# Optimization experiments

Measured on AMD Instinct MI355X. Metric: run time of the kernel, lower is better.

## Reference

```python
import jax, jax.numpy as jnp
import numpy as np
from jax import lax

B, H_IMG, W_IMG = 512, 812, 40
HID = 128
NUM_CLASSES = 12
LSTM_IN = 32 * ((W_IMG - 5) // 2 + 1)  # 32 channels * 18 = 576


def setup_inputs() -> dict:
    key = jax.random.key(0)
    ks = jax.random.split(key, 20)
    s = 0.05
    inp = {
        "x": jax.random.normal(ks[0], (B, 1, H_IMG, W_IMG), jnp.float32),
        "conv_w": jax.random.normal(ks[1], (32, 1, 20, 5), jnp.float32) * s,
        "conv_b": jax.random.normal(ks[2], (32,), jnp.float32) * s,
        "Wih0": jax.random.normal(ks[3], (4 * HID, LSTM_IN), jnp.float32) * s,
        "Whh0": jax.random.normal(ks[4], (4 * HID, HID), jnp.float32) * s,
        "bih0": jax.random.normal(ks[5], (4 * HID,), jnp.float32) * s,
        "bhh0": jax.random.normal(ks[6], (4 * HID,), jnp.float32) * s,
        "Wih1": jax.random.normal(ks[7], (4 * HID, HID), jnp.float32) * s,
        "Whh1": jax.random.normal(ks[8], (4 * HID, HID), jnp.float32) * s,
        "bih1": jax.random.normal(ks[9], (4 * HID,), jnp.float32) * s,
        "bhh1": jax.random.normal(ks[10], (4 * HID,), jnp.float32) * s,
        "W_att": jax.random.normal(ks[11], (HID, HID), jnp.float32) * s,
        "b_att": jax.random.normal(ks[12], (HID,), jnp.float32) * s,
        "v_att": jax.random.normal(ks[13], (HID,), jnp.float32) * s,
        "W1": jax.random.normal(ks[14], (64, HID), jnp.float32) * s,
        "b1": jax.random.normal(ks[15], (64,), jnp.float32) * s,
        "W2": jax.random.normal(ks[16], (NUM_CLASSES, 64), jnp.float32) * s,
        "b2": jax.random.normal(ks[17], (NUM_CLASSES,), jnp.float32) * s,
    }
    return inp


def _lstm_layer(seq, Wih, Whh, bih, bhh):
    # seq: (T, B, I); PyTorch gate order i, f, g, o
    T, Bn, _ = seq.shape
    Hd = Whh.shape[1]
    x_proj = jnp.einsum('tbi,gi->tbg', seq, Wih) + bih + bhh  # (T,B,4H)

    def step(carry, xg):
        h, c = carry
        g = xg + h @ Whh.T
        i, f, gg, o = jnp.split(g, 4, axis=-1)
        c = jax.nn.sigmoid(f) * c + jax.nn.sigmoid(i) * jnp.tanh(gg)
        h = jax.nn.sigmoid(o) * jnp.tanh(c)
        return (h, c), h

    init = (jnp.zeros((Bn, Hd), seq.dtype), jnp.zeros((Bn, Hd), seq.dtype))
    _, hs = lax.scan(step, init, x_proj)
    return hs  # (T,B,H)


def _forward(x, conv_w, conv_b, Wih0, Whh0, bih0, bhh0, Wih1, Whh1, bih1, bhh1,
             W_att, b_att, v_att, W1, b1, W2, b2):
    # Conv2d(1->32, k=(20,5), s=(8,2)) + ReLU
    y = lax.conv_general_dilated(x, conv_w, (8, 2), 'VALID',
                                 dimension_numbers=('NCHW', 'OIHW', 'NCHW'))
    y = jax.nn.relu(y + conv_b[None, :, None, None])  # (B,32,T,W')
    b, c, t, w = y.shape
    # permute(0,2,3,1).view(b,t,-1).permute(1,0,2) -> (T,B,W'*32)
    seq = jnp.transpose(y, (2, 0, 3, 1)).reshape(t, b, w * c)
    # 2-layer LSTM (inter-layer dropout=0.2 inactive at eval)
    h1 = _lstm_layer(seq, Wih0, Whh0, bih0, bhh0)
    h2 = _lstm_layer(h1, Wih1, Whh1, bih1, bhh1)
    # additive attention pooling over time
    squish = jnp.tanh(jnp.einsum('tbh,hk->tbk', h2, W_att) + b_att)  # (T,B,H)
    attn = jnp.einsum('tbh,h->tb', squish, v_att)                     # (T,B)
    w_att_n = jax.nn.softmax(attn, axis=0)                            # softmax over T
    pooled = jnp.einsum('tb,tbh->bh', w_att_n, h2)                    # (B,H)
    # dnn1 -> (dropout inactive at eval) -> output
    hdn = pooled @ W1.T + b1
    return hdn @ W2.T + b2  # (B,num_classes)


def reference(x, conv_w, conv_b, Wih0, Whh0, bih0, bhh0, Wih1, Whh1, bih1, bhh1,
              W_att, b_att, v_att, W1, b1, W2, b2):
    return _forward(x, conv_w, conv_b, Wih0, Whh0, bih0, bhh0, Wih1, Whh1,
                    bih1, bhh1, W_att, b_att, v_att, W1, b1, W2, b2)
```

## Files before the change

kernel.cpp:

```cpp
#include <hip/hip_runtime.h>
#include <stdint.h>


#define T_STEPS 100
#define BATCH   512
#define HIDD    128
#define GATES   512
#define LSTMIN  576
#define HIMG    812
#define WIMG    40

typedef __attribute__((ext_vector_type(8))) short bf16x8;
typedef __attribute__((ext_vector_type(4))) float f32x4;
typedef __attribute__((ext_vector_type(2))) __fp16 f16x2;

__device__ inline unsigned short f2bf(float f) {
  unsigned u = __float_as_uint(f);
  unsigned r = (u + 0x7fffu + ((u >> 16) & 1u)) >> 16;
  return (unsigned short)r;
}
__device__ inline float bf2f(unsigned short b) {
  return __uint_as_float(((unsigned)b) << 16);
}
__device__ inline float fsigm(float x) {
  float e = __expf(-x);
  return __builtin_amdgcn_rcpf(1.f + e);
}
__device__ inline float ftanh(float x) {
  float e = __expf(2.f * x);
  return (e - 1.f) * __builtin_amdgcn_rcpf(e + 1.f);
}
__device__ inline void lds_barrier() {
  asm volatile("s_waitcnt lgkmcnt(0)" ::: "memory");
  __builtin_amdgcn_s_barrier();
}
__device__ inline void full_barrier() {
  asm volatile("s_waitcnt vmcnt(0) lgkmcnt(0)" ::: "memory");
  __builtin_amdgcn_s_barrier();
}
__device__ inline void wait_flag(const int* fp, int need) {
  if ((threadIdx.x & 63) == 0) {
    int v = __hip_atomic_load(fp, __ATOMIC_ACQUIRE, __HIP_MEMORY_SCOPE_AGENT);
    while (v < need) {
      __builtin_amdgcn_s_sleep(2);
      v = __hip_atomic_load(fp, __ATOMIC_ACQUIRE, __HIP_MEMORY_SCOPE_AGENT);
    }
  }
}

__global__ void prep_kernel(const float* __restrict__ Wih0, const float* __restrict__ Whh0,
                            const float* __restrict__ Wih1, const float* __restrict__ Whh1,
                            const float* __restrict__ Watt, const float* __restrict__ convw,
                            const float* __restrict__ bih0, const float* __restrict__ bhh0,
                            const float* __restrict__ bih1, const float* __restrict__ bhh1,
                            unsigned short* __restrict__ wih0b, unsigned short* __restrict__ whh0b,
                            unsigned short* __restrict__ wih1b, unsigned short* __restrict__ whh1b,
                            unsigned short* __restrict__ wattb, f16x2* __restrict__ wpair,
                            float* __restrict__ bias0, float* __restrict__ bias1,
                            int* __restrict__ flags) {
  int tid = blockIdx.x * blockDim.x + threadIdx.x;
  int stride = gridDim.x * blockDim.x;
  for (int i = tid; i < GATES * LSTMIN; i += stride) wih0b[i] = f2bf(Wih0[i]);
  for (int i = tid; i < GATES * HIDD; i += stride) whh0b[i] = f2bf(Whh0[i]);
  for (int i = tid; i < GATES * HIDD; i += stride) wih1b[i] = f2bf(Wih1[i]);
  for (int i = tid; i < GATES * HIDD; i += stride) whh1b[i] = f2bf(Whh1[i]);
  for (int i = tid; i < HIDD * HIDD; i += stride) {
    int j = i >> 7, k = i & 127;
    wattb[i] = f2bf(Watt[k * HIDD + j]);
  }
  for (int i = tid; i < 50 * 32; i += stride) {
    int k2 = i >> 5, c = i & 31;
    int kh2 = k2 / 5, kw = k2 % 5;
    float lo = convw[c * 100 + (2 * kh2) * 5 + kw];
    float hi = convw[c * 100 + (2 * kh2 + 1) * 5 + kw];
    wpair[i] = __builtin_amdgcn_cvt_pkrtz(lo, hi);
  }
  for (int i = tid; i < GATES; i += stride) bias0[i] = bih0[i] + bhh0[i];
  for (int i = tid; i < GATES; i += stride) bias1[i] = bih1[i] + bhh1[i];
  for (int i = tid; i < 32; i += stride) flags[i] = 0;
}

__global__ __launch_bounds__(256) void conv_kernel(const float* __restrict__ x,
                                                   const f16x2* __restrict__ wpair,
                                                   const float* __restrict__ convb,
                                                   unsigned short* __restrict__ seq) {
  __shared__ f16x2 imgp[106 * WIMG];
  const int b = blockIdx.x;
  const int chunk = blockIdx.y;
  const int t0 = chunk * 25;
  const float* src = x + (size_t)b * (HIMG * WIMG) + (size_t)(8 * t0) * WIMG;
  for (int i = threadIdx.x; i < 106 * WIMG; i += 256) {
    int r2 = i / WIMG, c = i % WIMG;
    float lo = src[(2 * r2) * WIMG + c];
    float hi = src[(2 * r2 + 1) * WIMG + c];
    imgp[i] = __builtin_amdgcn_cvt_pkrtz(lo, hi);
  }
  __syncthreads();
  for (int p = threadIdx.x; p < 450; p += 256) {
    int tl = p / 18, wp = p % 18;
    int t = t0 + tl;
    float acc[32];
#pragma unroll
    for (int c = 0; c < 32; ++c) acc[c] = 0.f;
    const f16x2* ibase = imgp + (4 * tl) * WIMG + 2 * wp;
#pragma unroll 2
    for (int kh2 = 0; kh2 < 10; ++kh2) {
#pragma unroll
      for (int kw = 0; kw < 5; ++kw) {
        f16x2 iv = ibase[kh2 * WIMG + kw];
        const f16x2* wk = wpair + (kh2 * 5 + kw) * 32;
#pragma unroll
        for (int c = 0; c < 32; ++c)
          acc[c] = __builtin_amdgcn_fdot2(iv, wk[c], acc[c], false);
      }
    }
    unsigned short* o = seq + ((size_t)(t * BATCH + b)) * LSTMIN + wp * 32;
#pragma unroll
    for (int c = 0; c < 32; ++c) {
      float v = acc[c] + convb[c];
      o[c] = f2bf(v > 0.f ? v : 0.f);
    }
  }
}

template <int KDIM>
__global__ __launch_bounds__(256) void gemm_xp_kernel(const unsigned short* __restrict__ A,
                                                      const unsigned short* __restrict__ Bw,
                                                      const float* __restrict__ bias,
                                                      unsigned short* __restrict__ Xp) {
  __shared__ __align__(16) unsigned short As[128 * 32];
  __shared__ __align__(16) unsigned short Bs[128 * 32];
  const int tid = threadIdx.x;
  const int lane = tid & 63;
  const int w = tid >> 6;
  const int col16 = lane & 15;
  const int q = lane >> 4;
  const int n0 = blockIdx.x * 128;
  const int m0 = blockIdx.y * 128;
  const int wm = (w & 1) * 64;
  const int wn = (w >> 1) * 64;
  f32x4 acc[4][4] = {};
  const int r = tid >> 2;
  const int sw = ((tid & 3) ^ (r & 3)) * 8;
  const unsigned wslot = (unsigned)w * 512;
  const unsigned short* ga = A + (size_t)(m0 + r) * KDIM + sw;
  const unsigned short* gb = Bw + (size_t)(n0 + r) * KDIM + sw;
  for (int k0 = 0; k0 < KDIM; k0 += 32) {
    __syncthreads();
    __builtin_amdgcn_global_load_lds((const __attribute__((address_space(1))) void*)(ga + k0),
                                     (__attribute__((address_space(3))) void*)(As + wslot), 16, 0, 0);
    __builtin_amdgcn_global_load_lds((const __attribute__((address_space(1))) void*)(ga + k0 + (size_t)64 * KDIM),
                                     (__attribute__((address_space(3))) void*)(As + wslot + 2048), 16, 0, 0);
    __builtin_amdgcn_global_load_lds((const __attribute__((address_space(1))) void*)(gb + k0),
                                     (__attribute__((address_space(3))) void*)(Bs + wslot), 16, 0, 0);
    __builtin_amdgcn_global_load_lds((const __attribute__((address_space(1))) void*)(gb + k0 + (size_t)64 * KDIM),
                                     (__attribute__((address_space(3))) void*)(Bs + wslot + 2048), 16, 0, 0);
    __syncthreads();
    bf16x8 af[4], bv[4];
#pragma unroll
    for (int i = 0; i < 4; ++i) {
      int ra = wm + i * 16 + col16;
      af[i] = *(const bf16x8*)(As + ra * 32 + ((q ^ (ra & 3)) * 8));
      int rb2 = wn + i * 16 + col16;
      bv[i] = *(const bf16x8*)(Bs + rb2 * 32 + ((q ^ (rb2 & 3)) * 8));
    }
#pragma unroll
    for (int i = 0; i < 4; ++i)
#pragma unroll
      for (int j = 0; j < 4; ++j)
        acc[i][j] = __builtin_amdgcn_mfma_f32_16x16x32_bf16(af[i], bv[j], acc[i][j], 0, 0, 0);
  }
#pragma unroll
  for (int ct = 0; ct < 4; ++ct) {
    int n = n0 + wn + ct * 16 + col16;
    float bvv = bias[n];
    int wS = (n >> 4) & 7;
    int ntS = n >> 7;
    int c16S = n & 15;
#pragma unroll
    for (int rt = 0; rt < 4; ++rt) {
      int m = m0 + wm + rt * 16 + q * 4;
      int t = m >> 9;
      int bb = m & 511;
      int blk = bb >> 4;
      int r16 = bb & 15;
      ushort4 u;
      u.x = f2bf(acc[rt][ct][0] + bvv);
      u.y = f2bf(acc[rt][ct][1] + bvv);
      u.z = f2bf(acc[rt][ct][2] + bvv);
      u.w = f2bf(acc[rt][ct][3] + bvv);
      size_t tile = (((size_t)t * 32 + blk) * 8 + wS) * 4 + ntS;
      *(ushort4*)(Xp + tile * 256 + c16S * 16 + r16) = u;
    }
  }
}

__global__ __launch_bounds__(512, 2) void scan_pipe_kernel(
    const unsigned short* __restrict__ Xp0, const unsigned short* __restrict__ Whh0,
    const unsigned short* __restrict__ Wih1, const float* __restrict__ bias1,
    unsigned short* __restrict__ Xp1, const unsigned short* __restrict__ Whh1,
    unsigned short* __restrict__ hout, int* __restrict__ flags) {
  __shared__ __align__(16) unsigned short hb[2][16 * 136];
  const int tid = threadIdx.x;
  const int lane = tid & 63;
  const int w = tid >> 6;
  const int col16 = lane & 15;
  const int q = lane >> 4;
  const bool producer = blockIdx.x < 32;
  const int blk = producer ? (int)blockIdx.x : (int)blockIdx.x - 32;
  const int rb = blk * 16;
  const int hc = w * 16 + col16;
  const int srow = tid >> 5;
  const int scol = (tid & 31) * 4;
  int* flagp = flags + blk;

  if (producer) {
    bf16x8 bfrag[4][4], bfrag2[4][4];
    const unsigned short* xpb[4];
    unsigned short* xob[4];
    float biasn[4];
#pragma unroll
    for (int nt = 0; nt < 4; ++nt) {
      int cn = nt * HIDD + hc;
#pragma unroll
      for (int ks = 0; ks < 4; ++ks) {
        bfrag[nt][ks] = *(const bf16x8*)(Whh0 + (size_t)cn * HIDD + ks * 32 + q * 8);
        bfrag2[nt][ks] = *(const bf16x8*)(Wih1 + (size_t)cn * HIDD + ks * 32 + q * 8);
      }
      biasn[nt] = bias1[cn];
      size_t tile = (((size_t)blk) * 8 + w) * 4 + nt;
      xpb[nt] = Xp0 + tile * 256 + col16 * 16 + q * 4;
      xob[nt] = Xp1 + tile * 256 + col16 * 16 + q * 4;
    }
    uint2 xb[2][4];
#pragma unroll
    for (int nt = 0; nt < 4; ++nt) xb[0][nt] = *(const uint2*)(xpb[nt]);
#pragma unroll
    for (int nt = 0; nt < 4; ++nt) xb[1][nt] = *(const uint2*)(xpb[nt] + GATES * BATCH);
    for (int i = tid; i < 2 * 16 * 136; i += 512) hb[0][i] = 0;
    float cst[4] = {0.f, 0.f, 0.f, 0.f};
    lds_barrier();

#pragma unroll 4
    for (int t = 0; t < T_STEPS; ++t) {
      const int pb = (t & 1) ^ 1;
      bf16x8 af[4];
#pragma unroll
      for (int ks = 0; ks < 4; ++ks)
        af[ks] = *(const bf16x8*)(hb[pb] + col16 * 136 + ks * 32 + q * 8);
      const int s = t & 1;
      uint2 xv[4];
#pragma unroll
      for (int nt = 0; nt < 4; ++nt) xv[nt] = xb[s][nt];
      if (t + 2 < T_STEPS) {
#pragma unroll
        for (int nt = 0; nt < 4; ++nt)
          xb[s][nt] = *(const uint2*)(xpb[nt] + (size_t)(t + 2) * (GATES * BATCH));
      }
      f32x4 acc[4];
#pragma unroll
      for (int nt = 0; nt < 4; ++nt) {
        acc[nt][0] = __uint_as_float(xv[nt].x << 16);
        acc[nt][1] = __uint_as_float(xv[nt].x & 0xffff0000u);
        acc[nt][2] = __uint_as_float(xv[nt].y << 16);
        acc[nt][3] = __uint_as_float(xv[nt].y & 0xffff0000u);
      }
#pragma unroll
      for (int ks = 0; ks < 4; ++ks)
#pragma unroll
        for (int nt = 0; nt < 4; ++nt)
          acc[nt] = __builtin_amdgcn_mfma_f32_16x16x32_bf16(af[ks], bfrag[nt][ks], acc[nt], 0, 0, 0);
      f32x4 acc2[4];
#pragma unroll
      for (int nt = 0; nt < 4; ++nt) acc2[nt] = f32x4{0.f, 0.f, 0.f, 0.f};
#pragma unroll
      for (int ks = 0; ks < 4; ++ks)
#pragma unroll
        for (int nt = 0; nt < 4; ++nt)
          acc2[nt] = __builtin_amdgcn_mfma_f32_16x16x32_bf16(af[ks], bfrag2[nt][ks], acc2[nt], 0, 0, 0);
      unsigned short hv[4];
#pragma unroll
      for (int rr = 0; rr < 4; ++rr) {
        float pi = acc[0][rr], pf = acc[1][rr];
        float pg = acc[2][rr], po = acc[3][rr];
        float cc = fsigm(pf) * cst[rr] + fsigm(pi) * ftanh(pg);
        cst[rr] = cc;
        hv[rr] = f2bf(fsigm(po) * ftanh(cc));
      }
      if (t > 0) {
#pragma unroll
        for (int nt = 0; nt < 4; ++nt) {
          ushort4 u;
          u.x = f2bf(acc2[nt][0] + biasn[nt]);
          u.y = f2bf(acc2[nt][1] + biasn[nt]);
          u.z = f2bf(acc2[nt][2] + biasn[nt]);
          u.w = f2bf(acc2[nt][3] + biasn[nt]);
          *(ushort4*)(xob[nt] + (size_t)(t - 1) * (GATES * BATCH)) = u;
        }
      }
#pragma unroll
      for (int rr = 0; rr < 4; ++rr)
        hb[t & 1][(q * 4 + rr) * 136 + hc] = hv[rr];
      if ((t & 3) == 3) {
        full_barrier();
        if (tid == 0)
          __hip_atomic_store(flagp, t, __ATOMIC_RELEASE, __HIP_MEMORY_SCOPE_AGENT);
      } else {
        lds_barrier();
      }
    }
    bf16x8 af[4];
#pragma unroll
    for (int ks = 0; ks < 4; ++ks)
      af[ks] = *(const bf16x8*)(hb[(T_STEPS - 1) & 1] + col16 * 136 + ks * 32 + q * 8);
    f32x4 acc2[4];
#pragma unroll
    for (int nt = 0; nt < 4; ++nt) acc2[nt] = f32x4{0.f, 0.f, 0.f, 0.f};
#pragma unroll
    for (int ks = 0; ks < 4; ++ks)
#pragma unroll
      for (int nt = 0; nt < 4; ++nt)
        acc2[nt] = __builtin_amdgcn_mfma_f32_16x16x32_bf16(af[ks], bfrag2[nt][ks], acc2[nt], 0, 0, 0);
#pragma unroll
    for (int nt = 0; nt < 4; ++nt) {
      ushort4 u;
      u.x = f2bf(acc2[nt][0] + biasn[nt]);
      u.y = f2bf(acc2[nt][1] + biasn[nt]);
      u.z = f2bf(acc2[nt][2] + biasn[nt]);
      u.w = f2bf(acc2[nt][3] + biasn[nt]);
      *(ushort4*)(xob[nt] + (size_t)(T_STEPS - 1) * (GATES * BATCH)) = u;
    }
    full_barrier();
    if (tid == 0)
      __hip_atomic_store(flagp, 100, __ATOMIC_RELEASE, __HIP_MEMORY_SCOPE_AGENT);
  } else {
    bf16x8 bfrag[4][4];
    const unsigned short* xpb[4];
#pragma unroll
    for (int nt = 0; nt < 4; ++nt) {
      int cn = nt * HIDD + hc;
#pragma unroll
      for (int ks = 0; ks < 4; ++ks)
        bfrag[nt][ks] = *(const bf16x8*)(Whh1 + (size_t)cn * HIDD + ks * 32 + q * 8);
      size_t tile = (((size_t)blk) * 8 + w) * 4 + nt;
      xpb[nt] = Xp1 + tile * 256 + col16 * 16 + q * 4;
    }
    for (int i = tid; i < 2 * 16 * 136; i += 512) hb[0][i] = 0;
    wait_flag(flagp, 6);
    uint2 xb[2][4];
#pragma unroll
    for (int nt = 0; nt < 4; ++nt) xb[0][nt] = *(const uint2*)(xpb[nt]);
#pragma unroll
    for (int nt = 0; nt < 4; ++nt) xb[1][nt] = *(const uint2*)(xpb[nt] + GATES * BATCH);
    float cst[4] = {0.f, 0.f, 0.f, 0.f};
    lds_barrier();

#pragma unroll 4
    for (int t = 0; t < T_STEPS; ++t) {
      if (t > 0 && (t & 3) == 0) {
        int need = t + 6;
        if (need > 100) need = 100;
        wait_flag(flagp, need);
      }
      const int pb = (t & 1) ^ 1;
      bf16x8 af[4];
#pragma unroll
      for (int ks = 0; ks < 4; ++ks)
        af[ks] = *(const bf16x8*)(hb[pb] + col16 * 136 + ks * 32 + q * 8);
      if (t > 0) {
        ushort4 hx = *(const ushort4*)(hb[pb] + srow * 136 + scol);
        *(ushort4*)(hout + ((size_t)((t - 1) * BATCH) + rb + srow) * HIDD + scol) = hx;
      }
      const int s = t & 1;
      uint2 xv[4];
#pragma unroll
      for (int nt = 0; nt < 4; ++nt) xv[nt] = xb[s][nt];
      if (t + 2 < T_STEPS) {
#pragma unroll
        for (int nt = 0; nt < 4; ++nt)
          xb[s][nt] = *(const uint2*)(xpb[nt] + (size_t)(t + 2) * (GATES * BATCH));
      }
      f32x4 acc[4];
#pragma unroll
      for (int nt = 0; nt < 4; ++nt) {
        acc[nt][0] = __uint_as_float(xv[nt].x << 16);
        acc[nt][1] = __uint_as_float(xv[nt].x & 0xffff0000u);
        acc[nt][2] = __uint_as_float(xv[nt].y << 16);
        acc[nt][3] = __uint_as_float(xv[nt].y & 0xffff0000u);
      }
#pragma unroll
      for (int ks = 0; ks < 4; ++ks)
#pragma unroll
        for (int nt = 0; nt < 4; ++nt)
          acc[nt] = __builtin_amdgcn_mfma_f32_16x16x32_bf16(af[ks], bfrag[nt][ks], acc[nt], 0, 0, 0);
      unsigned short hv[4];
#pragma unroll
      for (int rr = 0; rr < 4; ++rr) {
        float pi = acc[0][rr], pf = acc[1][rr];
        float pg = acc[2][rr], po = acc[3][rr];
        float cc = fsigm(pf) * cst[rr] + fsigm(pi) * ftanh(pg);
        cst[rr] = cc;
        hv[rr] = f2bf(fsigm(po) * ftanh(cc));
      }
#pragma unroll
      for (int rr = 0; rr < 4; ++rr)
        hb[t & 1][(q * 4 + rr) * 136 + hc] = hv[rr];
      lds_barrier();
    }
    ushort4 hx = *(const ushort4*)(hb[(T_STEPS - 1) & 1] + srow * 136 + scol);
    *(ushort4*)(hout + ((size_t)((T_STEPS - 1) * BATCH) + rb + srow) * HIDD + scol) = hx;
  }
}

__global__ __launch_bounds__(256) void gemm_att_kernel(const unsigned short* __restrict__ A,
                                                       const unsigned short* __restrict__ Bw,
                                                       const float* __restrict__ b_att,
                                                       const float* __restrict__ v_att,
                                                       float* __restrict__ scores) {
  __shared__ __align__(16) unsigned short As[128 * 32];
  __shared__ __align__(16) unsigned short Bs[128 * 32];
  __shared__ float s_red[128];
  const int tid = threadIdx.x;
  const int lane = tid & 63;
  const int w = tid >> 6;
  const int col16 = lane & 15;
  const int q = lane >> 4;
  const int m0 = blockIdx.y * 128;
  const int wm = (w & 1) * 64;
  const int wn = (w >> 1) * 64;
  f32x4 acc[4][4] = {};
  const int r = tid >> 2;
  const int sw = ((tid & 3) ^ (r & 3)) * 8;
  const unsigned wslot = (unsigned)w * 512;
  const unsigned short* ga = A + (size_t)(m0 + r) * HIDD + sw;
  const unsigned short* gb = Bw + (size_t)r * HIDD + sw;
  for (int k0 = 0; k0 < HIDD; k0 += 32) {
    __syncthreads();
    __builtin_amdgcn_global_load_lds((const __attribute__((address_space(1))) void*)(ga + k0),
                                     (__attribute__((address_space(3))) void*)(As + wslot), 16, 0, 0);
    __builtin_amdgcn_global_load_lds((const __attribute__((address_space(1))) void*)(ga + k0 + (size_t)64 * HIDD),
                                     (__attribute__((address_space(3))) void*)(As + wslot + 2048), 16, 0, 0);
    __builtin_amdgcn_global_load_lds((const __attribute__((address_space(1))) void*)(gb + k0),
                                     (__attribute__((address_space(3))) void*)(Bs + wslot), 16, 0, 0);
    __builtin_amdgcn_global_load_lds((const __attribute__((address_space(1))) void*)(gb + k0 + (size_t)64 * HIDD),
                                     (__attribute__((address_space(3))) void*)(Bs + wslot + 2048), 16, 0, 0);
    __syncthreads();
    bf16x8 af[4], bv[4];
#pragma unroll
    for (int i = 0; i < 4; ++i) {
      int ra = wm + i * 16 + col16;
      af[i] = *(const bf16x8*)(As + ra * 32 + ((q ^ (ra & 3)) * 8));
      int rb2 = wn + i * 16 + col16;
      bv[i] = *(const bf16x8*)(Bs + rb2 * 32 + ((q ^ (rb2 & 3)) * 8));
    }
#pragma unroll
    for (int i = 0; i < 4; ++i)
#pragma unroll
      for (int j = 0; j < 4; ++j)
        acc[i][j] = __builtin_amdgcn_mfma_f32_16x16x32_bf16(af[i], bv[j], acc[i][j], 0, 0, 0);
  }
  if (tid < 128) s_red[tid] = 0.f;
  float rs[4][4];
#pragma unroll
  for (int rt = 0; rt < 4; ++rt)
#pragma unroll
    for (int rr = 0; rr < 4; ++rr) rs[rt][rr] = 0.f;
#pragma unroll
  for (int ct = 0; ct < 4; ++ct) {
    int n = wn + ct * 16 + col16;
    float bvv = b_att[n], vv = v_att[n];
#pragma unroll
    for (int rt = 0; rt < 4; ++rt)
#pragma unroll
      for (int rr = 0; rr < 4; ++rr) {
        float xv2 = acc[rt][ct][rr] + bvv;
        float e = __expf(2.f * xv2);
        rs[rt][rr] += vv * (e - 1.f) * __builtin_amdgcn_rcpf(e + 1.f);
      }
  }
#pragma unroll
  for (int off = 1; off < 16; off <<= 1)
#pragma unroll
    for (int rt = 0; rt < 4; ++rt)
#pragma unroll
      for (int rr = 0; rr < 4; ++rr) rs[rt][rr] += __shfl_xor(rs[rt][rr], off, 64);
  __syncthreads();
  if (col16 == 0) {
#pragma unroll
    for (int rt = 0; rt < 4; ++rt)
#pragma unroll
      for (int rr = 0; rr < 4; ++rr)
        atomicAdd(&s_red[wm + rt * 16 + q * 4 + rr], rs[rt][rr]);
  }
  __syncthreads();
  if (tid < 128) scores[m0 + tid] = s_red[tid];
}

__global__ __launch_bounds__(128) void final_kernel(const float* __restrict__ scores,
                                                    const unsigned short* __restrict__ h2,
                                                    const float* __restrict__ W1, const float* __restrict__ b1,
                                                    const float* __restrict__ W2, const float* __restrict__ b2,
                                                    float* __restrict__ out) {
  const int b = blockIdx.x;
  const int tid = threadIdx.x;
  __shared__ float wj[T_STEPS];
  __shared__ float red[128];
  __shared__ float pooled[128];
  __shared__ float hdn[64];
  float sv = (tid < T_STEPS) ? scores[tid * BATCH + b] : -1e30f;
  red[tid] = sv;
  __syncthreads();
#pragma unroll
  for (int off = 64; off > 0; off >>= 1) {
    if (tid < off) red[tid] = fmaxf(red[tid], red[tid + off]);
    __syncthreads();
  }
  float mx = red[0];
  __syncthreads();
  float ev = (tid < T_STEPS) ? __expf(sv - mx) : 0.f;
  red[tid] = ev;
  __syncthreads();
#pragma unroll
  for (int off = 64; off > 0; off >>= 1) {
    if (tid < off) red[tid] += red[tid + off];
    __syncthreads();
  }
  float inv = 1.0f / red[0];
  if (tid < T_STEPS) wj[tid] = ev * inv;
  __syncthreads();
  float p = 0.f;
  for (int t = 0; t < T_STEPS; ++t)
    p += wj[t] * bf2f(h2[((size_t)(t * BATCH + b)) * HIDD + tid]);
  pooled[tid] = p;
  __syncthreads();
  if (tid < 64) {
    float a = b1[tid];
    for (int h = 0; h < 128; ++h) a = fmaf(W1[tid * 128 + h], pooled[h], a);
    hdn[tid] = a;
  }
  __syncthreads();
  if (tid < 12) {
    float a = b2[tid];
    for (int j = 0; j < 64; ++j) a = fmaf(W2[tid * 64 + j], hdn[j], a);
    out[b * 12 + tid] = a;
  }
}

extern "C" void kernel_launch(void* const* d_in, const int* in_sizes, int n_in,
                              void* d_out, int out_size, void* d_ws, size_t ws_size,
                              hipStream_t stream) {
  (void)in_sizes; (void)n_in; (void)out_size; (void)ws_size;
  const float* x      = (const float*)d_in[0];
  const float* conv_w = (const float*)d_in[1];
  const float* conv_b = (const float*)d_in[2];
  const float* Wih0   = (const float*)d_in[3];
  const float* Whh0   = (const float*)d_in[4];
  const float* bih0   = (const float*)d_in[5];
  const float* bhh0   = (const float*)d_in[6];
  const float* Wih1   = (const float*)d_in[7];
  const float* Whh1   = (const float*)d_in[8];
  const float* bih1   = (const float*)d_in[9];
  const float* bhh1   = (const float*)d_in[10];
  const float* W_att  = (const float*)d_in[11];
  const float* b_att  = (const float*)d_in[12];
  const float* v_att  = (const float*)d_in[13];
  const float* W1     = (const float*)d_in[14];
  const float* b1     = (const float*)d_in[15];
  const float* W2     = (const float*)d_in[16];
  const float* b2     = (const float*)d_in[17];

  char* ws = (char*)d_ws;
  size_t off = 0;
  auto carve = [&](size_t bytes) { char* p = ws + off; off += (bytes + 255) & ~(size_t)255; return p; };
  unsigned short* seq    = (unsigned short*)carve((size_t)T_STEPS * BATCH * LSTMIN * 2);
  unsigned short* xp0    = (unsigned short*)carve((size_t)T_STEPS * GATES * BATCH * 2);
  unsigned short* h2     = (unsigned short*)carve((size_t)T_STEPS * BATCH * HIDD * 2);
  float*          scores = (float*)carve((size_t)T_STEPS * BATCH * 4);
  unsigned short* wih0b  = (unsigned short*)carve((size_t)GATES * LSTMIN * 2);
  unsigned short* whh0b  = (unsigned short*)carve((size_t)GATES * HIDD * 2);
  unsigned short* wih1b  = (unsigned short*)carve((size_t)GATES * HIDD * 2);
  unsigned short* whh1b  = (unsigned short*)carve((size_t)GATES * HIDD * 2);
  unsigned short* wattb  = (unsigned short*)carve((size_t)HIDD * HIDD * 2);
  f16x2*          wpair  = (f16x2*)carve(50 * 32 * 4);
  float*          bias0  = (float*)carve(GATES * 4);
  float*          bias1  = (float*)carve(GATES * 4);
  int*            flags  = (int*)carve(32 * 4);
  unsigned short* xp1 = seq;

  prep_kernel<<<256, 256, 0, stream>>>(Wih0, Whh0, Wih1, Whh1, W_att, conv_w,
                                       bih0, bhh0, bih1, bhh1,
                                       wih0b, whh0b, wih1b, whh1b, wattb, wpair,
                                       bias0, bias1, flags);
  conv_kernel<<<dim3(512, 4), 256, 0, stream>>>(x, wpair, conv_b, seq);
  gemm_xp_kernel<LSTMIN><<<dim3(4, 400), 256, 0, stream>>>(seq, wih0b, bias0, xp0);
  scan_pipe_kernel<<<64, 512, 0, stream>>>(xp0, whh0b, wih1b, bias1, xp1, whh1b, h2, flags);
  gemm_att_kernel<<<dim3(1, 400), 256, 0, stream>>>(h2, wattb, b_att, v_att, scores);
  final_kernel<<<512, 128, 0, stream>>>(scores, h2, W1, b1, W2, b2, (float*)d_out);
}
```

Measured before the change: 412.5 us.

## Defer layer-1 projection stores and relax producer-consumer flag synchronization

The producer now holds each step's layer-1 input projection in registers and stores it one step later as relaxed atomics. Its periodic barrier waits with vmcnt(4) instead of draining every outstanding global op, so the flag publish no longer stalls on the newest stores. Flag acquire and release become relaxed with compiler fences, the consumer lag grows by one step, packed bf16 conversion is used, and launch bounds drop to one block per SM. The relaxed ordering depends on the vmcnt counting being right and risks subtle memory-visibility races.

```diff
diff --git a/kernel.cpp b/kernel.cpp
--- a/kernel.cpp
+++ b/kernel.cpp
@@ -13,12 +13,21 @@
 typedef __attribute__((ext_vector_type(8))) short bf16x8;
 typedef __attribute__((ext_vector_type(4))) float f32x4;
 typedef __attribute__((ext_vector_type(2))) __fp16 f16x2;
+typedef unsigned long long ull;
 
 __device__ inline unsigned short f2bf(float f) {
   unsigned u = __float_as_uint(f);
   unsigned r = (u + 0x7fffu + ((u >> 16) & 1u)) >> 16;
   return (unsigned short)r;
 }
+__device__ inline unsigned pk_bf16(float a, float b) {
+#if __has_builtin(__builtin_amdgcn_cvt_pk_bf16_f32)
+  auto r = __builtin_amdgcn_cvt_pk_bf16_f32(a, b);
+  return __builtin_bit_cast(unsigned, r);
+#else
+  return (unsigned)f2bf(a) | ((unsigned)f2bf(b) << 16);
+#endif
+}
 __device__ inline float bf2f(unsigned short b) {
   return __uint_as_float(((unsigned)b) << 16);
 }
@@ -34,18 +43,12 @@
   asm volatile("s_waitcnt lgkmcnt(0)" ::: "memory");
   __builtin_amdgcn_s_barrier();
 }
-__device__ inline void full_barrier() {
-  asm volatile("s_waitcnt vmcnt(0) lgkmcnt(0)" ::: "memory");
-  __builtin_amdgcn_s_barrier();
-}
-__device__ inline void wait_flag(const int* fp, int need) {
+__device__ inline void wait_flag(int* fp, int need) {
   if ((threadIdx.x & 63) == 0) {
-    int v = __hip_atomic_load(fp, __ATOMIC_ACQUIRE, __HIP_MEMORY_SCOPE_AGENT);
-    while (v < need) {
+    while (__hip_atomic_load(fp, __ATOMIC_RELAXED, __HIP_MEMORY_SCOPE_AGENT) < need)
       __builtin_amdgcn_s_sleep(2);
-      v = __hip_atomic_load(fp, __ATOMIC_ACQUIRE, __HIP_MEMORY_SCOPE_AGENT);
-    }
-  }
+  }
+  asm volatile("" ::: "memory");
 }
 
 __global__ void prep_kernel(const float* __restrict__ Wih0, const float* __restrict__ Whh0,
@@ -195,7 +198,7 @@
   }
 }
 
-__global__ __launch_bounds__(512, 2) void scan_pipe_kernel(
+__global__ __launch_bounds__(512, 1) void scan_pipe_kernel(
     const unsigned short* __restrict__ Xp0, const unsigned short* __restrict__ Whh0,
     const unsigned short* __restrict__ Wih1, const float* __restrict__ bias1,
     unsigned short* __restrict__ Xp1, const unsigned short* __restrict__ Whh1,
@@ -217,7 +220,7 @@
   if (producer) {
     bf16x8 bfrag[4][4], bfrag2[4][4];
     const unsigned short* xpb[4];
-    unsigned short* xob[4];
+    ull* xob[4];
     float biasn[4];
 #pragma unroll
     for (int nt = 0; nt < 4; ++nt) {
@@ -230,7 +233,7 @@
       biasn[nt] = bias1[cn];
       size_t tile = (((size_t)blk) * 8 + w) * 4 + nt;
       xpb[nt] = Xp0 + tile * 256 + col16 * 16 + q * 4;
-      xob[nt] = Xp1 + tile * 256 + col16 * 16 + q * 4;
+      xob[nt] = (ull*)(Xp1 + tile * 256 + col16 * 16 + q * 4);
     }
     uint2 xb[2][4];
 #pragma unroll
@@ -239,24 +242,33 @@
     for (int nt = 0; nt < 4; ++nt) xb[1][nt] = *(const uint2*)(xpb[nt] + GATES * BATCH);
     for (int i = tid; i < 2 * 16 * 136; i += 512) hb[0][i] = 0;
     float cst[4] = {0.f, 0.f, 0.f, 0.f};
+    ull pend[4] = {0, 0, 0, 0};
     lds_barrier();
 
 #pragma unroll 4
     for (int t = 0; t < T_STEPS; ++t) {
+      if (t >= 2) {
+#pragma unroll
+        for (int nt = 0; nt < 4; ++nt)
+          __hip_atomic_store(xob[nt] + (size_t)(t - 2) * (GATES * BATCH / 4), pend[nt],
+                             __ATOMIC_RELAXED, __HIP_MEMORY_SCOPE_AGENT);
+      }
+      asm volatile("" ::: "memory");
+      const int s = t & 1;
+      uint2 xv[4];
+#pragma unroll
+      for (int nt = 0; nt < 4; ++nt) xv[nt] = xb[s][nt];
+      if (t + 2 < T_STEPS) {
+#pragma unroll
+        for (int nt = 0; nt < 4; ++nt)
+          xb[s][nt] = *(const uint2*)(xpb[nt] + (size_t)(t + 2) * (GATES * BATCH));
+      }
+      asm volatile("" ::: "memory");
       const int pb = (t & 1) ^ 1;
       bf16x8 af[4];
 #pragma unroll
       for (int ks = 0; ks < 4; ++ks)
         af[ks] = *(const bf16x8*)(hb[pb] + col16 * 136 + ks * 32 + q * 8);
-      const int s = t & 1;
-      uint2 xv[4];
-#pragma unroll
-      for (int nt = 0; nt < 4; ++nt) xv[nt] = xb[s][nt];
-      if (t + 2 < T_STEPS) {
-#pragma unroll
-        for (int nt = 0; nt < 4; ++nt)
-          xb[s][nt] = *(const uint2*)(xpb[nt] + (size_t)(t + 2) * (GATES * BATCH));
-      }
       f32x4 acc[4];
 #pragma unroll
       for (int nt = 0; nt < 4; ++nt) {
@@ -287,28 +299,27 @@
         cst[rr] = cc;
         hv[rr] = f2bf(fsigm(po) * ftanh(cc));
       }
-      if (t > 0) {
-#pragma unroll
-        for (int nt = 0; nt < 4; ++nt) {
-          ushort4 u;
-          u.x = f2bf(acc2[nt][0] + biasn[nt]);
-          u.y = f2bf(acc2[nt][1] + biasn[nt]);
-          u.z = f2bf(acc2[nt][2] + biasn[nt]);
-          u.w = f2bf(acc2[nt][3] + biasn[nt]);
-          *(ushort4*)(xob[nt] + (size_t)(t - 1) * (GATES * BATCH)) = u;
-        }
+#pragma unroll
+      for (int nt = 0; nt < 4; ++nt) {
+        unsigned lo = pk_bf16(acc2[nt][0] + biasn[nt], acc2[nt][1] + biasn[nt]);
+        unsigned hi = pk_bf16(acc2[nt][2] + biasn[nt], acc2[nt][3] + biasn[nt]);
+        pend[nt] = (ull)lo | ((ull)hi << 32);
       }
 #pragma unroll
       for (int rr = 0; rr < 4; ++rr)
         hb[t & 1][(q * 4 + rr) * 136 + hc] = hv[rr];
-      if ((t & 3) == 3) {
-        full_barrier();
+      if ((t & 3) == 3 && t < 99) {
+        asm volatile("s_waitcnt vmcnt(4) lgkmcnt(0)\ns_barrier" ::: "memory");
         if (tid == 0)
-          __hip_atomic_store(flagp, t, __ATOMIC_RELEASE, __HIP_MEMORY_SCOPE_AGENT);
+          __hip_atomic_store(flagp, t, __ATOMIC_RELAXED, __HIP_MEMORY_SCOPE_AGENT);
       } else {
         lds_barrier();
       }
     }
+#pragma unroll
+    for (int nt = 0; nt < 4; ++nt)
+      __hip_atomic_store(xob[nt] + (size_t)98 * (GATES * BATCH / 4), pend[nt],
+                         __ATOMIC_RELAXED, __HIP_MEMORY_SCOPE_AGENT);
     bf16x8 af[4];
 #pragma unroll
     for (int ks = 0; ks < 4; ++ks)
@@ -323,19 +334,18 @@
         acc2[nt] = __builtin_amdgcn_mfma_f32_16x16x32_bf16(af[ks], bfrag2[nt][ks], acc2[nt], 0, 0, 0);
 #pragma unroll
     for (int nt = 0; nt < 4; ++nt) {
-      ushort4 u;
-      u.x = f2bf(acc2[nt][0] + biasn[nt]);
-      u.y = f2bf(acc2[nt][1] + biasn[nt]);
-      u.z = f2bf(acc2[nt][2] + biasn[nt]);
-      u.w = f2bf(acc2[nt][3] + biasn[nt]);
-      *(ushort4*)(xob[nt] + (size_t)(T_STEPS - 1) * (GATES * BATCH)) = u;
-    }
-    full_barrier();
+      unsigned lo = pk_bf16(acc2[nt][0] + biasn[nt], acc2[nt][1] + biasn[nt]);
+      unsigned hi = pk_bf16(acc2[nt][2] + biasn[nt], acc2[nt][3] + biasn[nt]);
+      __hip_atomic_store(xob[nt] + (size_t)99 * (GATES * BATCH / 4),
+                         (ull)lo | ((ull)hi << 32),
+                         __ATOMIC_RELAXED, __HIP_MEMORY_SCOPE_AGENT);
+    }
+    asm volatile("s_waitcnt vmcnt(0) lgkmcnt(0)\ns_barrier" ::: "memory");
     if (tid == 0)
-      __hip_atomic_store(flagp, 100, __ATOMIC_RELEASE, __HIP_MEMORY_SCOPE_AGENT);
+      __hip_atomic_store(flagp, 101, __ATOMIC_RELAXED, __HIP_MEMORY_SCOPE_AGENT);
   } else {
     bf16x8 bfrag[4][4];
-    const unsigned short* xpb[4];
+    ull* xpb[4];
 #pragma unroll
     for (int nt = 0; nt < 4; ++nt) {
       int cn = nt * HIDD + hc;
@@ -343,23 +353,25 @@
       for (int ks = 0; ks < 4; ++ks)
         bfrag[nt][ks] = *(const bf16x8*)(Whh1 + (size_t)cn * HIDD + ks * 32 + q * 8);
       size_t tile = (((size_t)blk) * 8 + w) * 4 + nt;
-      xpb[nt] = Xp1 + tile * 256 + col16 * 16 + q * 4;
+      xpb[nt] = (ull*)(Xp1 + tile * 256 + col16 * 16 + q * 4);
     }
     for (int i = tid; i < 2 * 16 * 136; i += 512) hb[0][i] = 0;
-    wait_flag(flagp, 6);
-    uint2 xb[2][4];
-#pragma unroll
-    for (int nt = 0; nt < 4; ++nt) xb[0][nt] = *(const uint2*)(xpb[nt]);
-#pragma unroll
-    for (int nt = 0; nt < 4; ++nt) xb[1][nt] = *(const uint2*)(xpb[nt] + GATES * BATCH);
+    wait_flag(flagp, 7);
+    ull xb[2][4];
+#pragma unroll
+    for (int nt = 0; nt < 4; ++nt)
+      xb[0][nt] = __hip_atomic_load(xpb[nt], __ATOMIC_RELAXED, __HIP_MEMORY_SCOPE_AGENT);
+#pragma unroll
+    for (int nt = 0; nt < 4; ++nt)
+      xb[1][nt] = __hip_atomic_load(xpb[nt] + (GATES * BATCH / 4), __ATOMIC_RELAXED, __HIP_MEMORY_SCOPE_AGENT);
     float cst[4] = {0.f, 0.f, 0.f, 0.f};
     lds_barrier();
 
 #pragma unroll 4
     for (int t = 0; t < T_STEPS; ++t) {
       if (t > 0 && (t & 3) == 0) {
-        int need = t + 6;
-        if (need > 100) need = 100;
+        int need = t + 7;
+        if (need > 101) need = 101;
         wait_flag(flagp, need);
       }
       const int pb = (t & 1) ^ 1;
@@ -372,21 +384,24 @@
         *(ushort4*)(hout + ((size_t)((t - 1) * BATCH) + rb + srow) * HIDD + scol) = hx;
       }
       const int s = t & 1;
-      uint2 xv[4];
+      ull xv[4];
 #pragma unroll
       for (int nt = 0; nt < 4; ++nt) xv[nt] = xb[s][nt];
       if (t + 2 < T_STEPS) {
 #pragma unroll
         for (int nt = 0; nt < 4; ++nt)
-          xb[s][nt] = *(const uint2*)(xpb[nt] + (size_t)(t + 2) * (GATES * BATCH));
+          xb[s][nt] = __hip_atomic_load(xpb[nt] + (size_t)(t + 2) * (GATES * BATCH / 4),
+                                        __ATOMIC_RELAXED, __HIP_MEMORY_SCOPE_AGENT);
       }
       f32x4 acc[4];
 #pragma unroll
       for (int nt = 0; nt < 4; ++nt) {
-        acc[nt][0] = __uint_as_float(xv[nt].x << 16);
-        acc[nt][1] = __uint_as_float(xv[nt].x & 0xffff0000u);
-        acc[nt][2] = __uint_as_float(xv[nt].y << 16);
-        acc[nt][3] = __uint_as_float(xv[nt].y & 0xffff0000u);
+        unsigned lo = (unsigned)xv[nt];
+        unsigned hi = (unsigned)(xv[nt] >> 32);
+        acc[nt][0] = __uint_as_float(lo << 16);
+        acc[nt][1] = __uint_as_float(lo & 0xffff0000u);
+        acc[nt][2] = __uint_as_float(hi << 16);
+        acc[nt][3] = __uint_as_float(hi & 0xffff0000u);
       }
 #pragma unroll
       for (int ks = 0; ks < 4; ++ks)
```

Measured after the change: 412.6 us. About the same (+0.0%).
